# Kernel optimization log

Hardware: AMD Instinct MI355X
Metric: run time of the kernel (lower is better)

The kernel has to match this reference:

```python
import jax, jax.numpy as jnp
import numpy as np

N_HEADS = 16

def setup_inputs() -> dict:
    key = jax.random.key(0)
    k1, k2, k3 = jax.random.split(key, 3)
    B, T, C = 4, 2048, 1024
    x = jax.random.normal(k1, (B, T, C), dtype=jnp.float32)
    w_qkv = jax.random.normal(k2, (C, 3 * C), dtype=jnp.float32) * (1.0 / np.sqrt(C))
    w_out = jax.random.normal(k3, (C, C), dtype=jnp.float32) * (1.0 / np.sqrt(C))
    return {"x": x, "w_qkv": w_qkv, "w_out": w_out}

def reference(x, w_qkv, w_out):
    B, T, C = x.shape
    H = N_HEADS
    d_k = C // H
    qkv = x @ w_qkv                       # (B,T,3C)
    q, k, v = jnp.split(qkv, 3, axis=-1)
    # (B,H,T,d_k)
    q = q.reshape(B, T, H, d_k).transpose(0, 2, 1, 3)
    k = k.reshape(B, T, H, d_k).transpose(0, 2, 1, 3)
    v = v.reshape(B, T, H, d_k).transpose(0, 2, 1, 3)
    scale = 1.0 / np.sqrt(d_k)
    scores = jnp.einsum('bhqd,bhkd->bhqk', q, k) * scale  # (B,H,T,T)
    causal = jnp.triu(jnp.ones((T, T), dtype=bool), k=1)  # True = ignore
    scores = jnp.where(causal, -jnp.inf, scores)
    weights = jax.nn.softmax(scores, axis=-1)
    out = jnp.einsum('bhqk,bhkd->bhqd', weights, v)       # (B,H,T,d_k)
    out = out.transpose(0, 2, 1, 3).reshape(B, T, C)
    return out @ w_out
```

## Files before the change

### kernel.cpp

```cpp
#include <hip/hip_runtime.h>
#include <hip/hip_bf16.h>
#include <stdint.h>
#include <math.h>

typedef __bf16 bf16;
typedef __bf16 bf16x4 __attribute__((ext_vector_type(4)));
typedef __bf16 bf16x8 __attribute__((ext_vector_type(8)));
typedef float f32x4 __attribute__((ext_vector_type(4)));

#define BB 4
#define TT 2048
#define CC 1024
#define HH 16
#define DK 64

__device__ __forceinline__ void gl_lds16(const void* gsrc, void* ldst) {
    __builtin_amdgcn_global_load_lds(
        (__attribute__((address_space(1))) void*)(void*)(gsrc),
        (__attribute__((address_space(3))) void*)(ldst),
        16, 0, 0);
}

__global__ __launch_bounds__(256) void convert_x(
    const float* __restrict__ xin, bf16* __restrict__ xbf, int n) {
    const int i = (blockIdx.x * 256 + threadIdx.x) * 8;
    if (i >= n) return;
    const f32x4 a = *(const f32x4*)(xin + i);
    const f32x4 b = *(const f32x4*)(xin + i + 4);
    bf16x8 o;
#pragma unroll
    for (int j = 0; j < 4; ++j) { o[j] = (bf16)a[j]; o[j + 4] = (bf16)b[j]; }
    *(bf16x8*)(xbf + i) = o;
}

__global__ __launch_bounds__(256) void transpose_f32(
    const float* __restrict__ in, bf16* __restrict__ out, int R, int C) {
    __shared__ bf16 tile[32][33];
    const int c0 = blockIdx.x * 32, r0 = blockIdx.y * 32;
    const int tx = threadIdx.x & 31, ty = threadIdx.x >> 5;
#pragma unroll
    for (int i = 0; i < 32; i += 8)
        tile[ty + i][tx] = (bf16)in[(size_t)(r0 + ty + i) * C + c0 + tx];
    __syncthreads();
#pragma unroll
    for (int i = 0; i < 32; i += 8)
        out[(size_t)(c0 + ty + i) * R + r0 + tx] = tile[tx][ty + i];
}

template <int EPI>
__global__ __launch_bounds__(256) void gemm_bt(
    const bf16* __restrict__ A, const bf16* __restrict__ Bt,
    void* __restrict__ Cq, bf16* __restrict__ Kh, bf16* __restrict__ Vt,
    int M, int N, int K) {
    __shared__ bf16 As[128 * 32];
    __shared__ bf16 Bs[128 * 32];
    const int tid = threadIdx.x;
    const int w = tid >> 6, l = tid & 63;
    const int wm = w >> 1, wn = w & 1;
    const int m0 = blockIdx.y * 128, n0 = blockIdx.x * 128;
    const int lr4 = l >> 2, lc4 = (l & 3) * 8;
    const int lm = l & 15, lq = l >> 4;

    f32x4 acc[4][4] = {};

    for (int k0 = 0; k0 < K; k0 += 32) {
#pragma unroll
        for (int i = 0; i < 2; ++i) {
            const int j = w * 2 + i;
            gl_lds16(A + (size_t)(m0 + j * 16 + lr4) * K + k0 + lc4, As + j * 512);
            gl_lds16(Bt + (size_t)(n0 + j * 16 + lr4) * K + k0 + lc4, Bs + j * 512);
        }
        __syncthreads();
        bf16x8 af[4], bfr[4];
#pragma unroll
        for (int mi = 0; mi < 4; ++mi)
            af[mi] = *(const bf16x8*)(As + (wm * 64 + mi * 16 + lm) * 32 + lq * 8);
#pragma unroll
        for (int ni = 0; ni < 4; ++ni)
            bfr[ni] = *(const bf16x8*)(Bs + (wn * 64 + ni * 16 + lm) * 32 + lq * 8);
#pragma unroll
        for (int mi = 0; mi < 4; ++mi)
#pragma unroll
            for (int ni = 0; ni < 4; ++ni)
                acc[mi][ni] = __builtin_amdgcn_mfma_f32_16x16x32_bf16(
                    af[mi], bfr[ni], acc[mi][ni], 0, 0, 0);
        __syncthreads();
    }

    if (EPI == 0) {
#pragma unroll
        for (int mi = 0; mi < 4; ++mi) {
            const int row = m0 + wm * 64 + mi * 16 + lq * 4;
#pragma unroll
            for (int ni = 0; ni < 4; ++ni) {
                const int col = n0 + wn * 64 + ni * 16 + lm;
#pragma unroll
                for (int r = 0; r < 4; ++r)
                    ((float*)Cq)[(size_t)(row + r) * N + col] = acc[mi][ni][r];
            }
        }
    } else {
        bf16* Q = (bf16*)Cq;
#pragma unroll
        for (int ni = 0; ni < 4; ++ni) {
            const int c = n0 + wn * 64 + ni * 16 + lm;
            const int part = c >> 10;
            const int h = (c & 1023) >> 6;
            const int d = c & 63;
#pragma unroll
            for (int mi = 0; mi < 4; ++mi) {
                const int rowg = m0 + wm * 64 + mi * 16 + lq * 4;
#pragma unroll
                for (int r = 0; r < 4; ++r) {
                    const int rg = rowg + r;
                    const int b = rg >> 11, t = rg & 2047;
                    const bf16 v = (bf16)acc[mi][ni][r];
                    if (part == 0)
                        Q[((size_t)(b * HH + h) * TT + t) * DK + d] = v;
                    else if (part == 1)
                        Kh[((size_t)(b * HH + h) * TT + t) * DK + d] = v;
                    else
                        Vt[((size_t)(b * HH + h) * DK + d) * TT + t] = v;
                }
            }
        }
    }
}

#define PAD 72
__global__ __launch_bounds__(256) void attn_kernel(
    const bf16* __restrict__ Qh, const bf16* __restrict__ Kh,
    const bf16* __restrict__ Vt, bf16* __restrict__ O) {
    __shared__ bf16 Qs[64 * PAD];
    __shared__ bf16 Ks[64 * PAD];
    __shared__ bf16 Vs[64 * PAD];
    __shared__ bf16 Ps[64 * PAD];
    __shared__ float lS[64];
    const int tid = threadIdx.x, w = tid >> 6, l = tid & 63;
    const int lm = l & 15, lq = l >> 4;
    const int id = blockIdx.x + 16 * blockIdx.y;
    const int xcd = id & 7;
    const int bh = ((id >> 7) << 3) | xcd;
    const int p = (id >> 3) & 15;
    const int b = bh >> 4, h = bh & 15;
    const bf16* Qb = Qh + (size_t)bh * TT * DK;
    const bf16* Kb = Kh + (size_t)bh * TT * DK;
    const bf16* Vb = Vt + (size_t)bh * DK * TT;
    const int srow = tid >> 3, scol = (tid & 7) * 8;

    const float smul = 0.125f * 1.44269504088896340736f;

#pragma unroll
    for (int half = 0; half < 2; ++half) {
        const int qt = half ? (31 - p) : p;
        const int q0 = qt * 64;
        const int qg = q0 + w * 16 + lm;

#pragma unroll
        for (int i = 0; i < 2; ++i)
            *(bf16x8*)(Qs + (srow + i * 32) * PAD + scol) =
                *(const bf16x8*)(Qb + (size_t)(q0 + srow + i * 32) * DK + scol);
        __syncthreads();
        bf16x8 qf[2];
#pragma unroll
        for (int ks = 0; ks < 2; ++ks)
            qf[ks] = *(const bf16x8*)(Qs + (w * 16 + lm) * PAD + ks * 32 + lq * 8);

        f32x4 oacc[4] = {};
        float lrun = 0.f;

        for (int kt = 0; kt <= qt; ++kt) {
#pragma unroll
            for (int i = 0; i < 2; ++i) {
                *(bf16x8*)(Ks + (srow + i * 32) * PAD + scol) =
                    *(const bf16x8*)(Kb + (size_t)(kt * 64 + srow + i * 32) * DK + scol);
                *(bf16x8*)(Vs + (srow + i * 32) * PAD + scol) =
                    *(const bf16x8*)(Vb + (size_t)(srow + i * 32) * TT + kt * 64 + scol);
            }
            __syncthreads();

            f32x4 st[4] = {};
#pragma unroll
            for (int ks = 0; ks < 2; ++ks) {
#pragma unroll
                for (int nb = 0; nb < 4; ++nb) {
                    const bf16x8 kf =
                        *(const bf16x8*)(Ks + (nb * 16 + lm) * PAD + ks * 32 + lq * 8);
                    st[nb] = __builtin_amdgcn_mfma_f32_16x16x32_bf16(
                        kf, qf[ks], st[nb], 0, 0, 0);
                }
            }

            const bool diag = (kt == qt);
#pragma unroll
            for (int nb = 0; nb < 4; ++nb) {
                bf16x4 pk;
#pragma unroll
                for (int r = 0; r < 4; ++r) {
                    float arg = fmaf(st[nb][r], smul, -20.f);
                    if (diag) {
                        const int keyg = kt * 64 + nb * 16 + lq * 4 + r;
                        if (keyg > qg) arg = -1e30f;
                    }
                    const float pv = exp2f(arg);
                    lrun += pv;
                    pk[r] = (bf16)pv;
                }
                *(bf16x4*)(Ps + (w * 16 + lm) * PAD + nb * 16 + lq * 4) = pk;
            }
            __syncthreads();

#pragma unroll
            for (int ks = 0; ks < 2; ++ks) {
                const bf16x8 pf =
                    *(const bf16x8*)(Ps + (w * 16 + lm) * PAD + ks * 32 + lq * 8);
#pragma unroll
                for (int ni = 0; ni < 4; ++ni) {
                    const bf16x8 vf =
                        *(const bf16x8*)(Vs + (ni * 16 + lm) * PAD + ks * 32 + lq * 8);
                    oacc[ni] = __builtin_amdgcn_mfma_f32_16x16x32_bf16(
                        pf, vf, oacc[ni], 0, 0, 0);
                }
            }
            __syncthreads();
        }

        lrun += __shfl_xor(lrun, 16);
        lrun += __shfl_xor(lrun, 32);
        if (lq == 0) lS[w * 16 + lm] = lrun;
        __syncthreads();
        float linv[4];
#pragma unroll
        for (int r = 0; r < 4; ++r) linv[r] = 1.0f / lS[w * 16 + lq * 4 + r];
#pragma unroll
        for (int ni = 0; ni < 4; ++ni) {
            const int col = h * 64 + ni * 16 + lm;
#pragma unroll
            for (int r = 0; r < 4; ++r) {
                const int t = q0 + w * 16 + lq * 4 + r;
                O[((size_t)(b * TT + t)) * CC + col] = (bf16)(oacc[ni][r] * linv[r]);
            }
        }
        __syncthreads();
    }
}

extern "C" void kernel_launch(void* const* d_in, const int* in_sizes, int n_in,
                              void* d_out, int out_size, void* d_ws, size_t ws_size,
                              hipStream_t stream) {
    const float* x = (const float*)d_in[0];
    const float* w_qkv = (const float*)d_in[1];
    const float* w_out = (const float*)d_in[2];

    char* ws = (char*)d_ws;
    const size_t M1 = (size_t)1 << 20;
    bf16* Qh = (bf16*)(ws);
    bf16* Kh = (bf16*)(ws + 16 * M1);
    bf16* Vt = (bf16*)(ws + 32 * M1);
    bf16* Ob = (bf16*)(ws + 48 * M1);
    bf16* wqkvT = (bf16*)(ws + 64 * M1);
    bf16* woutT = (bf16*)(ws + 70 * M1);
    bf16* xbf = (bf16*)(ws + 72 * M1);

    convert_x<<<8388608 / 2048, 256, 0, stream>>>(x, xbf, 8388608);
    transpose_f32<<<dim3(3072 / 32, 1024 / 32), 256, 0, stream>>>(
        w_qkv, wqkvT, 1024, 3072);
    transpose_f32<<<dim3(1024 / 32, 1024 / 32), 256, 0, stream>>>(
        w_out, woutT, 1024, 1024);
    gemm_bt<1><<<dim3(3072 / 128, 8192 / 128), 256, 0, stream>>>(
        xbf, wqkvT, Qh, Kh, Vt, 8192, 3072, 1024);
    attn_kernel<<<dim3(16, BB * HH), 256, 0, stream>>>(Qh, Kh, Vt, Ob);
    gemm_bt<0><<<dim3(1024 / 128, 8192 / 128), 256, 0, stream>>>(
        Ob, woutT, d_out, nullptr, nullptr, 8192, 1024, 1024);
}
```

Baseline: 301.8 us.

## Use 128-row query tiles in attention and merge prep kernels into one launch

```diff
diff --git a/kernel.cpp b/kernel.cpp
--- a/kernel.cpp
+++ b/kernel.cpp
@@ -21,23 +21,35 @@
         16, 0, 0);
 }
 
-__global__ __launch_bounds__(256) void convert_x(
-    const float* __restrict__ xin, bf16* __restrict__ xbf, int n) {
-    const int i = (blockIdx.x * 256 + threadIdx.x) * 8;
-    if (i >= n) return;
-    const f32x4 a = *(const f32x4*)(xin + i);
-    const f32x4 b = *(const f32x4*)(xin + i + 4);
-    bf16x8 o;
-#pragma unroll
-    for (int j = 0; j < 4; ++j) { o[j] = (bf16)a[j]; o[j + 4] = (bf16)b[j]; }
-    *(bf16x8*)(xbf + i) = o;
-}
-
-__global__ __launch_bounds__(256) void transpose_f32(
-    const float* __restrict__ in, bf16* __restrict__ out, int R, int C) {
+__global__ __launch_bounds__(256) void prep(
+    const float* __restrict__ x, const float* __restrict__ wq,
+    const float* __restrict__ wo, bf16* __restrict__ xbf,
+    bf16* __restrict__ wqT, bf16* __restrict__ woT) {
     __shared__ bf16 tile[32][33];
-    const int c0 = blockIdx.x * 32, r0 = blockIdx.y * 32;
-    const int tx = threadIdx.x & 31, ty = threadIdx.x >> 5;
+    const int bid = blockIdx.x, tid = threadIdx.x;
+    if (bid < 4096) {
+        const int i = (bid * 256 + tid) * 8;
+        const f32x4 a = *(const f32x4*)(x + i);
+        const f32x4 b = *(const f32x4*)(x + i + 4);
+        bf16x8 o;
+#pragma unroll
+        for (int j = 0; j < 4; ++j) { o[j] = (bf16)a[j]; o[j + 4] = (bf16)b[j]; }
+        *(bf16x8*)(xbf + i) = o;
+        return;
+    }
+    const float* in;
+    bf16* out;
+    int R, C, c0, r0;
+    if (bid < 7168) {
+        const int tb = bid - 4096;
+        in = wq; out = wqT; R = 1024; C = 3072;
+        c0 = (tb % 96) * 32; r0 = (tb / 96) * 32;
+    } else {
+        const int tb = bid - 7168;
+        in = wo; out = woT; R = 1024; C = 1024;
+        c0 = (tb % 32) * 32; r0 = (tb / 32) * 32;
+    }
+    const int tx = tid & 31, ty = tid >> 5;
 #pragma unroll
     for (int i = 0; i < 32; i += 8)
         tile[ty + i][tx] = (bf16)in[(size_t)(r0 + ty + i) * C + c0 + tx];
@@ -131,17 +143,18 @@
 __global__ __launch_bounds__(256) void attn_kernel(
     const bf16* __restrict__ Qh, const bf16* __restrict__ Kh,
     const bf16* __restrict__ Vt, bf16* __restrict__ O) {
-    __shared__ bf16 Qs[64 * PAD];
+    __shared__ bf16 Qs[128 * PAD];
     __shared__ bf16 Ks[64 * PAD];
     __shared__ bf16 Vs[64 * PAD];
-    __shared__ bf16 Ps[64 * PAD];
-    __shared__ float lS[64];
+    __shared__ bf16 Ps[128 * PAD];
+    __shared__ float lS[128];
     const int tid = threadIdx.x, w = tid >> 6, l = tid & 63;
     const int lm = l & 15, lq = l >> 4;
-    const int id = blockIdx.x + 16 * blockIdx.y;
+    const int id = blockIdx.x;
     const int xcd = id & 7;
-    const int bh = ((id >> 7) << 3) | xcd;
-    const int p = (id >> 3) & 15;
+    const int j = id >> 3;
+    const int bh = xcd + 8 * (j >> 3);
+    const int p = j & 7;
     const int b = bh >> 4, h = bh & 15;
     const bf16* Qb = Qh + (size_t)bh * TT * DK;
     const bf16* Kb = Kh + (size_t)bh * TT * DK;
@@ -152,24 +165,27 @@
 
 #pragma unroll
     for (int half = 0; half < 2; ++half) {
-        const int qt = half ? (31 - p) : p;
-        const int q0 = qt * 64;
-        const int qg = q0 + w * 16 + lm;
-
-#pragma unroll
-        for (int i = 0; i < 2; ++i)
+        const int qt = half ? (15 - p) : p;
+        const int q0 = qt * 128;
+
+#pragma unroll
+        for (int i = 0; i < 4; ++i)
             *(bf16x8*)(Qs + (srow + i * 32) * PAD + scol) =
                 *(const bf16x8*)(Qb + (size_t)(q0 + srow + i * 32) * DK + scol);
         __syncthreads();
-        bf16x8 qf[2];
-#pragma unroll
-        for (int ks = 0; ks < 2; ++ks)
-            qf[ks] = *(const bf16x8*)(Qs + (w * 16 + lm) * PAD + ks * 32 + lq * 8);
-
-        f32x4 oacc[4] = {};
-        float lrun = 0.f;
-
-        for (int kt = 0; kt <= qt; ++kt) {
+        bf16x8 qf[2][2];
+#pragma unroll
+        for (int sub = 0; sub < 2; ++sub)
+#pragma unroll
+            for (int ks = 0; ks < 2; ++ks)
+                qf[sub][ks] = *(const bf16x8*)(Qs + (w * 32 + sub * 16 + lm) * PAD +
+                                               ks * 32 + lq * 8);
+
+        f32x4 oacc[2][4] = {};
+        float lrun[2] = {0.f, 0.f};
+
+        const int ktmax = 2 * qt + 1;
+        for (int kt = 0; kt <= ktmax; ++kt) {
 #pragma unroll
             for (int i = 0; i < 2; ++i) {
                 *(bf16x8*)(Ks + (srow + i * 32) * PAD + scol) =
@@ -179,66 +195,85 @@
             }
             __syncthreads();
 
-            f32x4 st[4] = {};
+            f32x4 st[2][4] = {};
 #pragma unroll
             for (int ks = 0; ks < 2; ++ks) {
 #pragma unroll
                 for (int nb = 0; nb < 4; ++nb) {
                     const bf16x8 kf =
                         *(const bf16x8*)(Ks + (nb * 16 + lm) * PAD + ks * 32 + lq * 8);
-                    st[nb] = __builtin_amdgcn_mfma_f32_16x16x32_bf16(
-                        kf, qf[ks], st[nb], 0, 0, 0);
-                }
-            }
-
-            const bool diag = (kt == qt);
-#pragma unroll
-            for (int nb = 0; nb < 4; ++nb) {
-                bf16x4 pk;
-#pragma unroll
-                for (int r = 0; r < 4; ++r) {
-                    float arg = fmaf(st[nb][r], smul, -20.f);
-                    if (diag) {
-                        const int keyg = kt * 64 + nb * 16 + lq * 4 + r;
-                        if (keyg > qg) arg = -1e30f;
+#pragma unroll
+                    for (int sub = 0; sub < 2; ++sub)
+                        st[sub][nb] = __builtin_amdgcn_mfma_f32_16x16x32_bf16(
+                            kf, qf[sub][ks], st[sub][nb], 0, 0, 0);
+                }
+            }
+
+            const bool diag = (kt >= 2 * qt);
+#pragma unroll
+            for (int sub = 0; sub < 2; ++sub) {
+                const int qg = q0 + w * 32 + sub * 16 + lm;
+#pragma unroll
+                for (int nb = 0; nb < 4; ++nb) {
+                    bf16x4 pk;
+#pragma unroll
+                    for (int r = 0; r < 4; ++r) {
+                        float arg = fmaf(st[sub][nb][r], smul, -20.f);
+                        if (diag) {
+                            const int keyg = kt * 64 + nb * 16 + lq * 4 + r;
+                            if (keyg > qg) arg = -1e30f;
+                        }
+                        const float pv = exp2f(arg);
+                        lrun[sub] += pv;
+                        pk[r] = (bf16)pv;
                     }
-                    const float pv = exp2f(arg);
-                    lrun += pv;
-                    pk[r] = (bf16)pv;
-                }
-                *(bf16x4*)(Ps + (w * 16 + lm) * PAD + nb * 16 + lq * 4) = pk;
-            }
-            __syncthreads();
+                    *(bf16x4*)(Ps + (w * 32 + sub * 16 + lm) * PAD + nb * 16 + lq * 4) =
+                        pk;
+                }
+            }
 
 #pragma unroll
             for (int ks = 0; ks < 2; ++ks) {
-                const bf16x8 pf =
-                    *(const bf16x8*)(Ps + (w * 16 + lm) * PAD + ks * 32 + lq * 8);
+                bf16x8 pf[2];
+#pragma unroll
+                for (int sub = 0; sub < 2; ++sub)
+                    pf[sub] = *(const bf16x8*)(Ps + (w * 32 + sub * 16 + lm) * PAD +
+                                               ks * 32 + lq * 8);
 #pragma unroll
                 for (int ni = 0; ni < 4; ++ni) {
                     const bf16x8 vf =
                         *(const bf16x8*)(Vs + (ni * 16 + lm) * PAD + ks * 32 + lq * 8);
-                    oacc[ni] = __builtin_amdgcn_mfma_f32_16x16x32_bf16(
-                        pf, vf, oacc[ni], 0, 0, 0);
+#pragma unroll
+                    for (int sub = 0; sub < 2; ++sub)
+                        oacc[sub][ni] = __builtin_amdgcn_mfma_f32_16x16x32_bf16(
+                            pf[sub], vf, oacc[sub][ni], 0, 0, 0);
                 }
             }
             __syncthreads();
         }
 
-        lrun += __shfl_xor(lrun, 16);
-        lrun += __shfl_xor(lrun, 32);
-        if (lq == 0) lS[w * 16 + lm] = lrun;
-        __syncthreads();
-        float linv[4];
-#pragma unroll
-        for (int r = 0; r < 4; ++r) linv[r] = 1.0f / lS[w * 16 + lq * 4 + r];
-#pragma unroll
-        for (int ni = 0; ni < 4; ++ni) {
-            const int col = h * 64 + ni * 16 + lm;
-#pragma unroll
-            for (int r = 0; r < 4; ++r) {
-                const int t = q0 + w * 16 + lq * 4 + r;
-                O[((size_t)(b * TT + t)) * CC + col] = (bf16)(oacc[ni][r] * linv[r]);
+#pragma unroll
+        for (int sub = 0; sub < 2; ++sub) {
+            lrun[sub] += __shfl_xor(lrun[sub], 16);
+            lrun[sub] += __shfl_xor(lrun[sub], 32);
+            if (lq == 0) lS[w * 32 + sub * 16 + lm] = lrun[sub];
+        }
+        __syncthreads();
+#pragma unroll
+        for (int sub = 0; sub < 2; ++sub) {
+            float linv[4];
+#pragma unroll
+            for (int r = 0; r < 4; ++r)
+                linv[r] = 1.0f / lS[w * 32 + sub * 16 + lq * 4 + r];
+#pragma unroll
+            for (int ni = 0; ni < 4; ++ni) {
+                const int col = h * 64 + ni * 16 + lm;
+#pragma unroll
+                for (int r = 0; r < 4; ++r) {
+                    const int t = q0 + w * 32 + sub * 16 + lq * 4 + r;
+                    O[((size_t)(b * TT + t)) * CC + col] =
+                        (bf16)(oacc[sub][ni][r] * linv[r]);
+                }
             }
         }
         __syncthreads();
@@ -262,14 +297,10 @@
     bf16* woutT = (bf16*)(ws + 70 * M1);
     bf16* xbf = (bf16*)(ws + 72 * M1);
 
-    convert_x<<<8388608 / 2048, 256, 0, stream>>>(x, xbf, 8388608);
-    transpose_f32<<<dim3(3072 / 32, 1024 / 32), 256, 0, stream>>>(
-        w_qkv, wqkvT, 1024, 3072);
-    transpose_f32<<<dim3(1024 / 32, 1024 / 32), 256, 0, stream>>>(
-        w_out, woutT, 1024, 1024);
+    prep<<<8192, 256, 0, stream>>>(x, w_qkv, w_out, xbf, wqkvT, woutT);
     gemm_bt<1><<<dim3(3072 / 128, 8192 / 128), 256, 0, stream>>>(
         xbf, wqkvT, Qh, Kh, Vt, 8192, 3072, 1024);
-    attn_kernel<<<dim3(16, BB * HH), 256, 0, stream>>>(Qh, Kh, Vt, Ob);
+    attn_kernel<<<512, 256, 0, stream>>>(Qh, Kh, Vt, Ob);
     gemm_bt<0><<<dim3(1024 / 128, 8192 / 128), 256, 0, stream>>>(
         Ob, woutT, d_out, nullptr, nullptr, 8192, 1024, 1024);
 }
```

Result: no change. 300.1 us (-0.6%).

## Double-buffer attention K/V with register prefetch, drop barriers, fuse prep kernels

Applied to the files above, without the earlier changes.

```diff
diff --git a/kernel.cpp b/kernel.cpp
--- a/kernel.cpp
+++ b/kernel.cpp
@@ -21,23 +21,35 @@
         16, 0, 0);
 }
 
-__global__ __launch_bounds__(256) void convert_x(
-    const float* __restrict__ xin, bf16* __restrict__ xbf, int n) {
-    const int i = (blockIdx.x * 256 + threadIdx.x) * 8;
-    if (i >= n) return;
-    const f32x4 a = *(const f32x4*)(xin + i);
-    const f32x4 b = *(const f32x4*)(xin + i + 4);
-    bf16x8 o;
-#pragma unroll
-    for (int j = 0; j < 4; ++j) { o[j] = (bf16)a[j]; o[j + 4] = (bf16)b[j]; }
-    *(bf16x8*)(xbf + i) = o;
-}
-
-__global__ __launch_bounds__(256) void transpose_f32(
-    const float* __restrict__ in, bf16* __restrict__ out, int R, int C) {
+__global__ __launch_bounds__(256) void prep(
+    const float* __restrict__ x, const float* __restrict__ wq,
+    const float* __restrict__ wo, bf16* __restrict__ xbf,
+    bf16* __restrict__ wqT, bf16* __restrict__ woT) {
     __shared__ bf16 tile[32][33];
-    const int c0 = blockIdx.x * 32, r0 = blockIdx.y * 32;
-    const int tx = threadIdx.x & 31, ty = threadIdx.x >> 5;
+    const int bid = blockIdx.x, tid = threadIdx.x;
+    if (bid < 4096) {
+        const int i = (bid * 256 + tid) * 8;
+        const f32x4 a = *(const f32x4*)(x + i);
+        const f32x4 b = *(const f32x4*)(x + i + 4);
+        bf16x8 o;
+#pragma unroll
+        for (int j = 0; j < 4; ++j) { o[j] = (bf16)a[j]; o[j + 4] = (bf16)b[j]; }
+        *(bf16x8*)(xbf + i) = o;
+        return;
+    }
+    const float* in;
+    bf16* out;
+    int R, C, c0, r0;
+    if (bid < 7168) {
+        const int tb = bid - 4096;
+        in = wq; out = wqT; R = 1024; C = 3072;
+        c0 = (tb % 96) * 32; r0 = (tb / 96) * 32;
+    } else {
+        const int tb = bid - 7168;
+        in = wo; out = woT; R = 1024; C = 1024;
+        c0 = (tb % 32) * 32; r0 = (tb / 32) * 32;
+    }
+    const int tx = tid & 31, ty = tid >> 5;
 #pragma unroll
     for (int i = 0; i < 32; i += 8)
         tile[ty + i][tx] = (bf16)in[(size_t)(r0 + ty + i) * C + c0 + tx];
@@ -128,20 +140,19 @@
 }
 
 #define PAD 72
-__global__ __launch_bounds__(256) void attn_kernel(
+__global__ __launch_bounds__(256, 3) void attn_kernel(
     const bf16* __restrict__ Qh, const bf16* __restrict__ Kh,
     const bf16* __restrict__ Vt, bf16* __restrict__ O) {
-    __shared__ bf16 Qs[64 * PAD];
-    __shared__ bf16 Ks[64 * PAD];
-    __shared__ bf16 Vs[64 * PAD];
+    __shared__ bf16 Ks[2][64 * PAD];
+    __shared__ bf16 Vs[2][64 * PAD];
     __shared__ bf16 Ps[64 * PAD];
-    __shared__ float lS[64];
     const int tid = threadIdx.x, w = tid >> 6, l = tid & 63;
     const int lm = l & 15, lq = l >> 4;
-    const int id = blockIdx.x + 16 * blockIdx.y;
+    const int id = blockIdx.x;
     const int xcd = id & 7;
-    const int bh = ((id >> 7) << 3) | xcd;
-    const int p = (id >> 3) & 15;
+    const int rest = id >> 3;
+    const int bh = xcd + 8 * (rest >> 4);
+    const int p = rest & 15;
     const int b = bh >> 4, h = bh & 15;
     const bf16* Qb = Qh + (size_t)bh * TT * DK;
     const bf16* Kb = Kh + (size_t)bh * TT * DK;
@@ -149,22 +160,27 @@
     const int srow = tid >> 3, scol = (tid & 7) * 8;
 
     const float smul = 0.125f * 1.44269504088896340736f;
+    const int qts[2] = {p, 31 - p};
+
+    bf16x8 kreg[2], vreg[2];
+#pragma unroll
+    for (int i = 0; i < 2; ++i) {
+        kreg[i] = *(const bf16x8*)(Kb + (size_t)(srow + i * 32) * DK + scol);
+        vreg[i] = *(const bf16x8*)(Vb + (size_t)(srow + i * 32) * TT + scol);
+    }
+    int buf = 0;
 
 #pragma unroll
     for (int half = 0; half < 2; ++half) {
-        const int qt = half ? (31 - p) : p;
+        const int qt = qts[half];
         const int q0 = qt * 64;
         const int qg = q0 + w * 16 + lm;
 
-#pragma unroll
-        for (int i = 0; i < 2; ++i)
-            *(bf16x8*)(Qs + (srow + i * 32) * PAD + scol) =
-                *(const bf16x8*)(Qb + (size_t)(q0 + srow + i * 32) * DK + scol);
-        __syncthreads();
         bf16x8 qf[2];
 #pragma unroll
         for (int ks = 0; ks < 2; ++ks)
-            qf[ks] = *(const bf16x8*)(Qs + (w * 16 + lm) * PAD + ks * 32 + lq * 8);
+            qf[ks] = *(const bf16x8*)(Qb + (size_t)(q0 + w * 16 + lm) * DK +
+                                      ks * 32 + lq * 8);
 
         f32x4 oacc[4] = {};
         float lrun = 0.f;
@@ -172,20 +188,33 @@
         for (int kt = 0; kt <= qt; ++kt) {
 #pragma unroll
             for (int i = 0; i < 2; ++i) {
-                *(bf16x8*)(Ks + (srow + i * 32) * PAD + scol) =
-                    *(const bf16x8*)(Kb + (size_t)(kt * 64 + srow + i * 32) * DK + scol);
-                *(bf16x8*)(Vs + (srow + i * 32) * PAD + scol) =
-                    *(const bf16x8*)(Vb + (size_t)(srow + i * 32) * TT + kt * 64 + scol);
+                *(bf16x8*)(Ks[buf] + (srow + i * 32) * PAD + scol) = kreg[i];
+                *(bf16x8*)(Vs[buf] + (srow + i * 32) * PAD + scol) = vreg[i];
             }
             __syncthreads();
 
+            {
+                int nkt = -1;
+                if (kt < qt) nkt = kt + 1;
+                else if (half == 0) nkt = 0;
+                if (nkt >= 0) {
+#pragma unroll
+                    for (int i = 0; i < 2; ++i) {
+                        kreg[i] = *(const bf16x8*)(
+                            Kb + (size_t)(nkt * 64 + srow + i * 32) * DK + scol);
+                        vreg[i] = *(const bf16x8*)(
+                            Vb + (size_t)(srow + i * 32) * TT + nkt * 64 + scol);
+                    }
+                }
+            }
+
             f32x4 st[4] = {};
 #pragma unroll
             for (int ks = 0; ks < 2; ++ks) {
 #pragma unroll
                 for (int nb = 0; nb < 4; ++nb) {
-                    const bf16x8 kf =
-                        *(const bf16x8*)(Ks + (nb * 16 + lm) * PAD + ks * 32 + lq * 8);
+                    const bf16x8 kf = *(const bf16x8*)(Ks[buf] + (nb * 16 + lm) * PAD +
+                                                       ks * 32 + lq * 8);
                     st[nb] = __builtin_amdgcn_mfma_f32_16x16x32_bf16(
                         kf, qf[ks], st[nb], 0, 0, 0);
                 }
@@ -208,7 +237,6 @@
                 }
                 *(bf16x4*)(Ps + (w * 16 + lm) * PAD + nb * 16 + lq * 4) = pk;
             }
-            __syncthreads();
 
 #pragma unroll
             for (int ks = 0; ks < 2; ++ks) {
@@ -216,22 +244,20 @@
                     *(const bf16x8*)(Ps + (w * 16 + lm) * PAD + ks * 32 + lq * 8);
 #pragma unroll
                 for (int ni = 0; ni < 4; ++ni) {
-                    const bf16x8 vf =
-                        *(const bf16x8*)(Vs + (ni * 16 + lm) * PAD + ks * 32 + lq * 8);
+                    const bf16x8 vf = *(const bf16x8*)(Vs[buf] + (ni * 16 + lm) * PAD +
+                                                       ks * 32 + lq * 8);
                     oacc[ni] = __builtin_amdgcn_mfma_f32_16x16x32_bf16(
                         pf, vf, oacc[ni], 0, 0, 0);
                 }
             }
-            __syncthreads();
+            buf ^= 1;
         }
 
         lrun += __shfl_xor(lrun, 16);
         lrun += __shfl_xor(lrun, 32);
-        if (lq == 0) lS[w * 16 + lm] = lrun;
-        __syncthreads();
         float linv[4];
 #pragma unroll
-        for (int r = 0; r < 4; ++r) linv[r] = 1.0f / lS[w * 16 + lq * 4 + r];
+        for (int r = 0; r < 4; ++r) linv[r] = 1.0f / __shfl(lrun, lq * 4 + r);
 #pragma unroll
         for (int ni = 0; ni < 4; ++ni) {
             const int col = h * 64 + ni * 16 + lm;
@@ -241,7 +267,6 @@
                 O[((size_t)(b * TT + t)) * CC + col] = (bf16)(oacc[ni][r] * linv[r]);
             }
         }
-        __syncthreads();
     }
 }
 
@@ -262,14 +287,10 @@
     bf16* woutT = (bf16*)(ws + 70 * M1);
     bf16* xbf = (bf16*)(ws + 72 * M1);
 
-    convert_x<<<8388608 / 2048, 256, 0, stream>>>(x, xbf, 8388608);
-    transpose_f32<<<dim3(3072 / 32, 1024 / 32), 256, 0, stream>>>(
-        w_qkv, wqkvT, 1024, 3072);
-    transpose_f32<<<dim3(1024 / 32, 1024 / 32), 256, 0, stream>>>(
-        w_out, woutT, 1024, 1024);
+    prep<<<8192, 256, 0, stream>>>(x, w_qkv, w_out, xbf, wqkvT, woutT);
     gemm_bt<1><<<dim3(3072 / 128, 8192 / 128), 256, 0, stream>>>(
         xbf, wqkvT, Qh, Kh, Vt, 8192, 3072, 1024);
-    attn_kernel<<<dim3(16, BB * HH), 256, 0, stream>>>(Qh, Kh, Vt, Ob);
+    attn_kernel<<<1024, 256, 0, stream>>>(Qh, Kh, Vt, Ob);
     gemm_bt<0><<<dim3(1024 / 128, 8192 / 128), 256, 0, stream>>>(
-        Ob, woutT, d_out, nullptr, nullptr, 8192, 1024, 1024);
-}
+        Ob, woutT, (float*)d_out, nullptr, nullptr, 8192, 1024, 1024);
+}
```

After: 286.3 us. -5.2%, faster.
